# Performance work log

Hardware: AMD Instinct MI355X
Metric: run time of the kernel (lower is better)

Reference implementation:

```python
import jax, jax.numpy as jnp
import numpy as np

S, B, D, E, F = 2048, 2, 1024, 8, 4096


def setup_inputs() -> dict:
    key = jax.random.key(0)
    ks = jax.random.split(key, 6)
    x = jax.random.normal(ks[0], (S, B, D), dtype=jnp.float32)
    w_switch = jax.random.normal(ks[1], (D, E), dtype=jnp.float32) / np.sqrt(D)
    b_switch = jnp.zeros((E,), dtype=jnp.float32)
    w1 = jax.random.normal(ks[2], (E, D, F), dtype=jnp.float32) / np.sqrt(D)
    b1 = jnp.zeros((E, F), dtype=jnp.float32)
    w2 = jax.random.normal(ks[3], (E, F, D), dtype=jnp.float32) / np.sqrt(F)
    b2 = jnp.zeros((E, D), dtype=jnp.float32)
    return {"x": x, "w_switch": w_switch, "b_switch": b_switch,
            "w1": w1, "b1": b1, "w2": w2, "b2": b2}


def reference(x, w_switch, b_switch, w1, b1, w2, b2):
    # x: [S, B, D] -> tokens [N, D]
    s, b, d = x.shape
    n_experts = w1.shape[0]
    xf = x.reshape(-1, d)                                    # [N, D]
    route_prob = jax.nn.softmax(xf @ w_switch + b_switch, axis=-1)  # [N, E]
    route_prob_max = jnp.max(route_prob, axis=-1)            # [N]
    routes = jnp.argmax(route_prob, axis=-1)                 # [N] int
    # is_scale_prob=True: scale token by its routing probability before FFN
    xs = xf * route_prob_max[:, None]                        # [N, D]
    # Per-expert FFN evaluated densely (drop_tokens=False => every token kept),
    # then each token selects its routed expert's output.
    h = jax.nn.relu(jnp.einsum('nd,edf->enf', xs, w1) + b1[:, None, :])  # [E, N, F]
    y = jnp.einsum('enf,efd->end', h, w2) + b2[:, None, :]               # [E, N, D]
    n = xf.shape[0]
    out = y[routes, jnp.arange(n)]                           # [N, D]
    counts = jnp.zeros((n_experts,), dtype=jnp.float32).at[routes].add(1.0)
    n_dropped = jnp.zeros((), dtype=jnp.int32)               # drop_tokens=False
    return out.reshape(s, b, d), counts, route_prob.sum(0), n_dropped
```

## Files before the change

### kernel.cpp

```cpp
#include <hip/hip_runtime.h>
#include <hip/hip_bf16.h>

#define NTOK 4096
#define DDIM 1024
#define NEXP 8
#define FDIM 4096
#define MAXTILES 40

typedef __attribute__((ext_vector_type(4))) float f32x4;
typedef __attribute__((ext_vector_type(8))) short bf16x8;
typedef __attribute__((ext_vector_type(8))) unsigned short u16x8;

#define GLDS(g, l) __builtin_amdgcn_global_load_lds( \
    (const __attribute__((address_space(1))) unsigned int*)(g), \
    (__attribute__((address_space(3))) unsigned int*)(l), 16, 0, 0)

__global__ __launch_bounds__(256) void route_kernel(
    const float* __restrict__ x,
    const float* __restrict__ w_switch,
    const float* __restrict__ b_switch,
    __hip_bfloat16* __restrict__ xs,
    int* __restrict__ amax_arr,
    float* __restrict__ partial)
{
    const int tid = threadIdx.x;
    const int wave = tid >> 6, lane = tid & 63;
    __shared__ float pr[4][16];

    float wacc[16];
#pragma unroll
    for (int j = 0; j < 16; j++) wacc[j] = 0.0f;

    for (int i = 0; i < 4; i++) {
        const int n = blockIdx.x * 16 + wave * 4 + i;
        const float4* xr = (const float4*)(x + (size_t)n * DDIM);
        float4 xv[4];
#pragma unroll
        for (int j = 0; j < 4; j++) xv[j] = xr[lane + j * 64];

        float acc[NEXP];
#pragma unroll
        for (int e = 0; e < NEXP; e++) acc[e] = 0.0f;
#pragma unroll
        for (int j = 0; j < 4; j++) {
            const int dbase = (lane + j * 64) * 4;
#pragma unroll
            for (int c = 0; c < 4; c++) {
                const float4* wr = (const float4*)(w_switch + (size_t)(dbase + c) * NEXP);
                float4 w0 = wr[0], w1 = wr[1];
                float xvc = ((const float*)&xv[j])[c];
                acc[0] += xvc * w0.x; acc[1] += xvc * w0.y;
                acc[2] += xvc * w0.z; acc[3] += xvc * w0.w;
                acc[4] += xvc * w1.x; acc[5] += xvc * w1.y;
                acc[6] += xvc * w1.z; acc[7] += xvc * w1.w;
            }
        }
#pragma unroll
        for (int e = 0; e < NEXP; e++) {
            float v = acc[e];
#pragma unroll
            for (int off = 32; off > 0; off >>= 1) v += __shfl_xor(v, off, 64);
            acc[e] = v;
        }
        float mx = -1e30f;
#pragma unroll
        for (int e = 0; e < NEXP; e++) {
            acc[e] += b_switch[e];
            mx = fmaxf(mx, acc[e]);
        }
        float sum = 0.0f;
#pragma unroll
        for (int e = 0; e < NEXP; e++) { acc[e] = __expf(acc[e] - mx); sum += acc[e]; }
        float inv = 1.0f / sum;
        float pmax = -1.0f; int amax = 0;
#pragma unroll
        for (int e = 0; e < NEXP; e++) {
            float p = acc[e] * inv;
            acc[e] = p;
            if (p > pmax) { pmax = p; amax = e; }
        }
#pragma unroll
        for (int e = 0; e < NEXP; e++) {
            wacc[e] += acc[e];
            wacc[8 + e] += (amax == e) ? 1.0f : 0.0f;
        }
        if (lane == 0) amax_arr[n] = amax;
#pragma unroll
        for (int j = 0; j < 4; j++) {
            ushort4 pk;
            __hip_bfloat16* pp = (__hip_bfloat16*)&pk;
            pp[0] = __float2bfloat16(xv[j].x * pmax);
            pp[1] = __float2bfloat16(xv[j].y * pmax);
            pp[2] = __float2bfloat16(xv[j].z * pmax);
            pp[3] = __float2bfloat16(xv[j].w * pmax);
            *(ushort4*)(xs + (size_t)n * DDIM + (lane + j * 64) * 4) = pk;
        }
    }
    if (lane == 0) {
#pragma unroll
        for (int j = 0; j < 16; j++) pr[wave][j] = wacc[j];
    }
    __syncthreads();
    if (tid < 16)
        partial[blockIdx.x * 16 + tid] = pr[0][tid] + pr[1][tid] + pr[2][tid] + pr[3][tid];
}

__global__ __launch_bounds__(1024) void bucket_kernel(
    const int* __restrict__ amax_arr, int* __restrict__ bucket, int* __restrict__ ecnt)
{
    const int e = blockIdx.x;
    __shared__ int ctr;
    if (threadIdx.x == 0) ctr = 0;
    __syncthreads();
    const int lane = threadIdx.x & 63;
    for (int c = 0; c < NTOK; c += 1024) {
        int t = c + threadIdx.x;
        bool my = (amax_arr[t] == e);
        unsigned long long mask = __ballot(my);
        int cnt = __popcll(mask);
        int base = 0;
        if (lane == 0 && cnt) base = atomicAdd(&ctr, cnt);
        base = __shfl(base, 0, 64);
        if (my) {
            int rank = __popcll(mask & ((1ull << lane) - 1ull));
            bucket[e * NTOK + base + rank] = t;
        }
    }
    __syncthreads();
    if (threadIdx.x == 0) ecnt[e] = ctr;
}

__global__ __launch_bounds__(256) void finalize_table_kernel(
    const float* __restrict__ partial, const int* __restrict__ ecnt,
    float* __restrict__ out_tail, int* __restrict__ table)
{
    __shared__ float red[16][16];
    const int j = threadIdx.x & 15, g = threadIdx.x >> 4;
    float s = 0.0f;
    for (int k = 0; k < 16; k++) s += partial[(size_t)(g + k * 16) * 16 + j];
    red[g][j] = s;
    __syncthreads();
    if (threadIdx.x < 16) {
        float t = 0.0f;
        for (int k = 0; k < 16; k++) t += red[k][threadIdx.x];
        int dst = (threadIdx.x < 8) ? (8 + threadIdx.x) : (threadIdx.x - 8);
        out_tail[dst] = t;
    }
    if (threadIdx.x == 16) out_tail[16] = 0.0f;
    if (threadIdx.x == 0) {
        int idx = 0;
        for (int e = 0; e < NEXP; e++) {
            int cnt = ecnt[e];
            for (int m0 = 0; m0 < cnt; m0 += 128) table[idx++] = (e << 16) | m0;
        }
        for (; idx < MAXTILES; idx++) table[idx] = -1;
    }
}

template <int R, int C>
__global__ __launch_bounds__(256) void transpose_kernel(
    const float* __restrict__ in, __hip_bfloat16* __restrict__ outp)
{
    const int e = blockIdx.z;
    const int r0 = blockIdx.y * 64, c0 = blockIdx.x * 64;
    __shared__ __hip_bfloat16 t[64 * 65];
    const int tid = threadIdx.x;
    const int ri = tid >> 4, c4 = (tid & 15) * 4;
    const float* src = in + ((size_t)e * R + r0) * C + c0;
#pragma unroll
    for (int rr = 0; rr < 4; rr++) {
        int r = ri + rr * 16;
        float4 v = *(const float4*)(src + (size_t)r * C + c4);
        t[r * 65 + c4 + 0] = __float2bfloat16(v.x);
        t[r * 65 + c4 + 1] = __float2bfloat16(v.y);
        t[r * 65 + c4 + 2] = __float2bfloat16(v.z);
        t[r * 65 + c4 + 3] = __float2bfloat16(v.w);
    }
    __syncthreads();
    const int co = tid >> 2, m = tid & 3;
    u16x8 v0, v1;
#pragma unroll
    for (int idx = 0; idx < 8; idx++)
        ((unsigned short*)&v0)[idx] = *(const unsigned short*)&t[(m * 16 + idx) * 65 + co];
#pragma unroll
    for (int idx = 0; idx < 8; idx++)
        ((unsigned short*)&v1)[idx] = *(const unsigned short*)&t[(m * 16 + idx + 8) * 65 + co];
    __hip_bfloat16* dst = outp + ((size_t)e * C + c0 + co) * R + r0 + m * 16;
    *(u16x8*)(dst) = v0;
    *(u16x8*)(dst + 8) = v1;
}

template <int MODE, int K, int NN, int KS, int NX>
__device__ __forceinline__ void gemm_body(
    const __hip_bfloat16* __restrict__ A,
    const __hip_bfloat16* __restrict__ Bt,
    const float* __restrict__ bias,
    const int* __restrict__ bucket,
    const int* __restrict__ ecnt,
    const int* __restrict__ table,
    void* __restrict__ Out)
{
    const int bid = blockIdx.x;
    const int xcd = bid & 7;
    const int q = bid >> 3;
    const int x = q % NX;
    const int yk = (q / NX) % (MAXTILES / 8);
    const int z = q / (NX * (MAXTILES / 8));
    const int y = xcd + 8 * yk;

    const int entry = table[y];
    if (entry < 0) return;
    const int e = entry >> 16;
    const int m0 = entry & 0xffff;
    const int cnt = ecnt[e];
    const int n0 = x * 128;
    const int kbase = (K / KS) * z;

    __shared__ __align__(16) __hip_bfloat16 Asm[128 * 32];
    __shared__ __align__(16) __hip_bfloat16 Bsm[128 * 32];
    __shared__ int toks[128];

    const int tid = threadIdx.x;
    if (tid < 128) {
        int r = m0 + tid;
        toks[tid] = bucket[e * NTOK + (r < cnt ? r : cnt - 1)];
    }
    __syncthreads();

    const int wave = tid >> 6, lane = tid & 63;
    const int r = lane & 15, kq = lane >> 4;
    const int g0 = 2 * wave, g1 = 2 * wave + 1;

    const __hip_bfloat16* pA0 = A + (size_t)toks[g0 * 16 + r] * K + kbase + kq * 8;
    const __hip_bfloat16* pA1 = A + (size_t)toks[g1 * 16 + r] * K + kbase + kq * 8;
    const __hip_bfloat16* pB0 = Bt + ((size_t)e * NN + n0 + g0 * 16 + r) * K + kbase + kq * 8;
    const __hip_bfloat16* pB1 = Bt + ((size_t)e * NN + n0 + g1 * 16 + r) * K + kbase + kq * 8;
    char* lA0 = (char*)Asm + g0 * 1024;
    char* lA1 = (char*)Asm + g1 * 1024;
    char* lB0 = (char*)Bsm + g0 * 1024;
    char* lB1 = (char*)Bsm + g1 * 1024;

    const int wm = wave & 1, wn = wave >> 1;
    f32x4 acc[4][4];
#pragma unroll
    for (int t = 0; t < 4; t++)
#pragma unroll
        for (int u = 0; u < 4; u++) acc[t][u] = (f32x4){0.f, 0.f, 0.f, 0.f};

    for (int k0 = 0; k0 < K / KS; k0 += 32) {
        GLDS(pA0, lA0); GLDS(pA1, lA1);
        GLDS(pB0, lB0); GLDS(pB1, lB1);
        pA0 += 32; pA1 += 32; pB0 += 32; pB1 += 32;
        __syncthreads();
        bf16x8 a[4], b[4];
#pragma unroll
        for (int t = 0; t < 4; t++)
            a[t] = *(const bf16x8*)((const char*)Asm + (wm * 4 + t) * 1024 + lane * 16);
#pragma unroll
        for (int u = 0; u < 4; u++)
            b[u] = *(const bf16x8*)((const char*)Bsm + (wn * 4 + u) * 1024 + lane * 16);
#pragma unroll
        for (int t = 0; t < 4; t++)
#pragma unroll
            for (int u = 0; u < 4; u++)
                acc[t][u] = __builtin_amdgcn_mfma_f32_16x16x32_bf16(a[t], b[u], acc[t][u], 0, 0, 0);
        __syncthreads();
    }

    const int quad = lane >> 4, l15 = lane & 15;
    float bv[4];
#pragma unroll
    for (int u = 0; u < 4; u++) {
        if (MODE == 0)
            bv[u] = bias[(size_t)e * NN + n0 + wn * 64 + u * 16 + l15];
        else
            bv[u] = (z == 0) ? bias[(size_t)e * NN + n0 + wn * 64 + u * 16 + l15] : 0.0f;
    }
#pragma unroll
    for (int t = 0; t < 4; t++) {
#pragma unroll
        for (int rr = 0; rr < 4; rr++) {
            int row = wm * 64 + t * 16 + quad * 4 + rr;
            if (m0 + row < cnt) {
                int tok = toks[row];
#pragma unroll
                for (int u = 0; u < 4; u++) {
                    int col = n0 + wn * 64 + u * 16 + l15;
                    float v = acc[t][u][rr] + bv[u];
                    if (MODE == 0) {
                        v = fmaxf(v, 0.0f);
                        ((__hip_bfloat16*)Out)[(size_t)tok * NN + col] = __float2bfloat16(v);
                    } else {
                        unsafeAtomicAdd(&((float*)Out)[(size_t)tok * NN + col], v);
                    }
                }
            }
        }
    }
}

__global__ __launch_bounds__(256) void gemm_ffn1(
    const __hip_bfloat16* __restrict__ A, const __hip_bfloat16* __restrict__ Bt,
    const float* __restrict__ bias, const int* __restrict__ bucket,
    const int* __restrict__ ecnt, const int* __restrict__ table, void* __restrict__ Out)
{
    gemm_body<0, DDIM, FDIM, 1, FDIM / 128>(A, Bt, bias, bucket, ecnt, table, Out);
}

__global__ __launch_bounds__(256) void gemm_ffn2(
    const __hip_bfloat16* __restrict__ A, const __hip_bfloat16* __restrict__ Bt,
    const float* __restrict__ bias, const int* __restrict__ bucket,
    const int* __restrict__ ecnt, const int* __restrict__ table, void* __restrict__ Out)
{
    gemm_body<1, FDIM, DDIM, 2, DDIM / 128>(A, Bt, bias, bucket, ecnt, table, Out);
}

extern "C" void kernel_launch(void* const* d_in, const int* in_sizes, int n_in,
                              void* d_out, int out_size, void* d_ws, size_t ws_size,
                              hipStream_t stream) {
    const float* x        = (const float*)d_in[0];
    const float* w_switch = (const float*)d_in[1];
    const float* b_switch = (const float*)d_in[2];
    const float* w1       = (const float*)d_in[3];
    const float* b1       = (const float*)d_in[4];
    const float* w2       = (const float*)d_in[5];
    const float* b2       = (const float*)d_in[6];

    float* out = (float*)d_out;
    float* out_tail = out + (size_t)NTOK * DDIM;

    char* ws = (char*)d_ws;
    __hip_bfloat16* xs = (__hip_bfloat16*)(ws);
    __hip_bfloat16* h  = (__hip_bfloat16*)(ws + 8388608ull);
    __hip_bfloat16* wt = (__hip_bfloat16*)(ws + 41943040ull);
    int* bucket        = (int*)(ws + 109051904ull);
    int* amax_arr      = (int*)(ws + 109182976ull);
    float* partial     = (float*)(ws + 109199360ull);
    int* ecnt          = (int*)(ws + 109215744ull);
    int* table         = (int*)(ws + 109215776ull);

    hipMemsetAsync(out, 0, (size_t)NTOK * DDIM * sizeof(float), stream);

    hipLaunchKernelGGL(route_kernel, dim3(256), dim3(256), 0, stream,
                       x, w_switch, b_switch, xs, amax_arr, partial);
    hipLaunchKernelGGL(bucket_kernel, dim3(NEXP), dim3(1024), 0, stream,
                       amax_arr, bucket, ecnt);
    hipLaunchKernelGGL(finalize_table_kernel, dim3(1), dim3(256), 0, stream,
                       partial, ecnt, out_tail, table);

    hipLaunchKernelGGL((transpose_kernel<DDIM, FDIM>), dim3(FDIM / 64, DDIM / 64, NEXP),
                       dim3(256), 0, stream, w1, wt);
    hipLaunchKernelGGL(gemm_ffn1, dim3((FDIM / 128) * MAXTILES), dim3(256), 0, stream,
                       xs, wt, b1, bucket, ecnt, table, (void*)h);

    hipLaunchKernelGGL((transpose_kernel<FDIM, DDIM>), dim3(DDIM / 64, FDIM / 64, NEXP),
                       dim3(256), 0, stream, w2, wt);
    hipLaunchKernelGGL(gemm_ffn2, dim3((DDIM / 128) * MAXTILES * 2), dim3(256), 0, stream,
                       h, wt, b2, bucket, ecnt, table, (void*)out);
}
```

Before: 515.3 us.

## Triple-buffer LDS tiles with async global_load_lds prefetch in expert GEMM

Replaces the single-buffered load/sync/compute loop in the grouped expert GEMM with a three-stage ring of LDS buffers. Loads for step t+2 are issued before computing step t, with manual vmcnt waits and raw s_barrier instead of two __syncthreads per step. LDS fragment reads use inline ds_read_b128 with immediate offsets. This hides global load latency behind MFMA work, at the cost of tripling LDS usage per block, which may reduce occupancy, and of relying on fragile hand-counted waitcnts.

```diff
diff --git a/kernel.cpp b/kernel.cpp
--- a/kernel.cpp
+++ b/kernel.cpp
@@ -14,6 +14,10 @@
 #define GLDS(g, l) __builtin_amdgcn_global_load_lds( \
     (const __attribute__((address_space(1))) unsigned int*)(g), \
     (__attribute__((address_space(3))) unsigned int*)(l), 16, 0, 0)
+
+#define LDSOFF(p) ((unsigned)(unsigned long long)(__attribute__((address_space(3))) char*)(p))
+
+#define DSR(dst, a, o) asm volatile("ds_read_b128 %0, %1 offset:" o : "=v"(dst) : "v"(a))
 
 __global__ __launch_bounds__(256) void route_kernel(
     const float* __restrict__ x,
@@ -216,8 +220,8 @@
     const int n0 = x * 128;
     const int kbase = (K / KS) * z;
 
-    __shared__ __align__(16) __hip_bfloat16 Asm[128 * 32];
-    __shared__ __align__(16) __hip_bfloat16 Bsm[128 * 32];
+    __shared__ __align__(16) __hip_bfloat16 Asm[3][128 * 32];
+    __shared__ __align__(16) __hip_bfloat16 Bsm[3][128 * 32];
     __shared__ int toks[128];
 
     const int tid = threadIdx.x;
@@ -229,42 +233,68 @@
 
     const int wave = tid >> 6, lane = tid & 63;
     const int r = lane & 15, kq = lane >> 4;
-    const int g0 = 2 * wave, g1 = 2 * wave + 1;
+    const int g0 = 2 * wave;
 
     const __hip_bfloat16* pA0 = A + (size_t)toks[g0 * 16 + r] * K + kbase + kq * 8;
-    const __hip_bfloat16* pA1 = A + (size_t)toks[g1 * 16 + r] * K + kbase + kq * 8;
+    const __hip_bfloat16* pA1 = A + (size_t)toks[(g0 + 1) * 16 + r] * K + kbase + kq * 8;
     const __hip_bfloat16* pB0 = Bt + ((size_t)e * NN + n0 + g0 * 16 + r) * K + kbase + kq * 8;
-    const __hip_bfloat16* pB1 = Bt + ((size_t)e * NN + n0 + g1 * 16 + r) * K + kbase + kq * 8;
-    char* lA0 = (char*)Asm + g0 * 1024;
-    char* lA1 = (char*)Asm + g1 * 1024;
-    char* lB0 = (char*)Bsm + g0 * 1024;
-    char* lB1 = (char*)Bsm + g1 * 1024;
+    const __hip_bfloat16* pB1 = Bt + ((size_t)e * NN + n0 + (g0 + 1) * 16 + r) * K + kbase + kq * 8;
 
     const int wm = wave & 1, wn = wave >> 1;
+    const unsigned aBase = LDSOFF((char*)Asm) + wm * 4096 + lane * 16;
+    const unsigned bBase = LDSOFF((char*)Bsm) + wn * 4096 + lane * 16;
+
     f32x4 acc[4][4];
 #pragma unroll
     for (int t = 0; t < 4; t++)
 #pragma unroll
         for (int u = 0; u < 4; u++) acc[t][u] = (f32x4){0.f, 0.f, 0.f, 0.f};
 
-    for (int k0 = 0; k0 < K / KS; k0 += 32) {
-        GLDS(pA0, lA0); GLDS(pA1, lA1);
-        GLDS(pB0, lB0); GLDS(pB1, lB1);
+    constexpr int NSTEP = (K / KS) / 32;
+    static_assert(NSTEP >= 3, "pipeline needs >=3 K-steps");
+
+    auto stage = [&](int b) {
+        char* la = (char*)Asm + b * 8192 + g0 * 1024;
+        char* lb = (char*)Bsm + b * 8192 + g0 * 1024;
+        GLDS(pA0, la); GLDS(pA1, la + 1024);
+        GLDS(pB0, lb); GLDS(pB1, lb + 1024);
         pA0 += 32; pA1 += 32; pB0 += 32; pB1 += 32;
-        __syncthreads();
-        bf16x8 a[4], b[4];
-#pragma unroll
-        for (int t = 0; t < 4; t++)
-            a[t] = *(const bf16x8*)((const char*)Asm + (wm * 4 + t) * 1024 + lane * 16);
-#pragma unroll
-        for (int u = 0; u < 4; u++)
-            b[u] = *(const bf16x8*)((const char*)Bsm + (wn * 4 + u) * 1024 + lane * 16);
-#pragma unroll
-        for (int t = 0; t < 4; t++)
+    };
+
+    stage(0);
+    stage(1);
+    asm volatile("s_waitcnt vmcnt(4)");
+    __builtin_amdgcn_s_barrier();
+
+    int cb = 0, sb = 2;
+    for (int t = 0; t < NSTEP; ++t) {
+        if (t + 2 < NSTEP) stage(sb);
+
+        const unsigned aA = aBase + cb * 8192;
+        const unsigned aB = bBase + cb * 8192;
+        bf16x8 af[4], bf_[4];
+        DSR(af[0], aA, "0");    DSR(af[1], aA, "1024");
+        DSR(af[2], aA, "2048"); DSR(af[3], aA, "3072");
+        DSR(bf_[0], aB, "0");    DSR(bf_[1], aB, "1024");
+        DSR(bf_[2], aB, "2048"); DSR(bf_[3], aB, "3072");
+        asm volatile("s_waitcnt lgkmcnt(0)");
+        __builtin_amdgcn_sched_barrier(0);
+
+#pragma unroll
+        for (int t4 = 0; t4 < 4; t4++)
 #pragma unroll
             for (int u = 0; u < 4; u++)
-                acc[t][u] = __builtin_amdgcn_mfma_f32_16x16x32_bf16(a[t], b[u], acc[t][u], 0, 0, 0);
-        __syncthreads();
+                acc[t4][u] = __builtin_amdgcn_mfma_f32_16x16x32_bf16(af[t4], bf_[u], acc[t4][u], 0, 0, 0);
+
+        if (t + 2 < NSTEP) {
+            asm volatile("s_waitcnt vmcnt(4)");
+            __builtin_amdgcn_s_barrier();
+        } else if (t + 1 < NSTEP) {
+            asm volatile("s_waitcnt vmcnt(0)");
+            __builtin_amdgcn_s_barrier();
+        }
+        cb = (cb == 2) ? 0 : cb + 1;
+        sb = (sb == 2) ? 0 : sb + 1;
     }
 
     const int quad = lane >> 4, l15 = lane & 15;
```

Result: no change. 513.0 us (-0.4%).

## Double GEMM K-tile to 64, row-major LDS staging, split-K 4 for FFN2

Applied to the files above, without the earlier changes.

The grouped expert GEMMs now stage a 64-wide K slice per iteration instead of 32. Each LDS buffer is laid out as 128 rows of 128 bytes, and the MFMA loop runs two sub-steps per barrier pair, which halves the number of __syncthreads per K. The second FFN GEMM raises split-K from 2 to 4 to put more blocks on the device, at the cost of more atomic adds into the fp32 output. Launch bounds now request 4 blocks per SM. The row-major LDS reads at a 128-byte stride may cause bank conflicts that the old fragment-ordered layout avoided.

```diff
diff --git a/kernel.cpp b/kernel.cpp
--- a/kernel.cpp
+++ b/kernel.cpp
@@ -216,8 +216,8 @@
     const int n0 = x * 128;
     const int kbase = (K / KS) * z;
 
-    __shared__ __align__(16) __hip_bfloat16 Asm[128 * 32];
-    __shared__ __align__(16) __hip_bfloat16 Bsm[128 * 32];
+    __shared__ __align__(16) __hip_bfloat16 Asm[128 * 64];
+    __shared__ __align__(16) __hip_bfloat16 Bsm[128 * 64];
     __shared__ int toks[128];
 
     const int tid = threadIdx.x;
@@ -228,42 +228,51 @@
     __syncthreads();
 
     const int wave = tid >> 6, lane = tid & 63;
-    const int r = lane & 15, kq = lane >> 4;
-    const int g0 = 2 * wave, g1 = 2 * wave + 1;
-
-    const __hip_bfloat16* pA0 = A + (size_t)toks[g0 * 16 + r] * K + kbase + kq * 8;
-    const __hip_bfloat16* pA1 = A + (size_t)toks[g1 * 16 + r] * K + kbase + kq * 8;
-    const __hip_bfloat16* pB0 = Bt + ((size_t)e * NN + n0 + g0 * 16 + r) * K + kbase + kq * 8;
-    const __hip_bfloat16* pB1 = Bt + ((size_t)e * NN + n0 + g1 * 16 + r) * K + kbase + kq * 8;
-    char* lA0 = (char*)Asm + g0 * 1024;
-    char* lA1 = (char*)Asm + g1 * 1024;
-    char* lB0 = (char*)Bsm + g0 * 1024;
-    char* lB1 = (char*)Bsm + g1 * 1024;
+    const int srow = lane >> 3;
+    const int scol = (lane & 7) * 16;
+
+    const char* pA[4];
+#pragma unroll
+    for (int i = 0; i < 4; i++)
+        pA[i] = (const char*)(A + (size_t)toks[wave * 32 + i * 8 + srow] * K + kbase) + scol;
+    const char* pB = (const char*)(Bt + ((size_t)e * NN + n0 + wave * 32 + srow) * K + kbase) + scol;
 
     const int wm = wave & 1, wn = wave >> 1;
+    const int r16 = lane & 15, kq16 = lane >> 4;
+
     f32x4 acc[4][4];
 #pragma unroll
     for (int t = 0; t < 4; t++)
 #pragma unroll
         for (int u = 0; u < 4; u++) acc[t][u] = (f32x4){0.f, 0.f, 0.f, 0.f};
 
-    for (int k0 = 0; k0 < K / KS; k0 += 32) {
-        GLDS(pA0, lA0); GLDS(pA1, lA1);
-        GLDS(pB0, lB0); GLDS(pB1, lB1);
-        pA0 += 32; pA1 += 32; pB0 += 32; pB1 += 32;
+    for (int k0 = 0; k0 < K / KS; k0 += 64) {
+#pragma unroll
+        for (int i = 0; i < 4; i++) {
+            GLDS(pA[i], (char*)Asm + (wave * 32 + i * 8) * 128 + lane * 16);
+            GLDS(pB + (size_t)i * 8 * K * 2, (char*)Bsm + (wave * 32 + i * 8) * 128 + lane * 16);
+            pA[i] += 128;
+        }
+        pB += 128;
         __syncthreads();
-        bf16x8 a[4], b[4];
-#pragma unroll
-        for (int t = 0; t < 4; t++)
-            a[t] = *(const bf16x8*)((const char*)Asm + (wm * 4 + t) * 1024 + lane * 16);
-#pragma unroll
-        for (int u = 0; u < 4; u++)
-            b[u] = *(const bf16x8*)((const char*)Bsm + (wn * 4 + u) * 1024 + lane * 16);
-#pragma unroll
-        for (int t = 0; t < 4; t++)
+
+#pragma unroll
+        for (int ksub = 0; ksub < 2; ksub++) {
+            bf16x8 a[4], b[4];
+#pragma unroll
+            for (int t = 0; t < 4; t++)
+                a[t] = *(const bf16x8*)((const char*)Asm +
+                        (wm * 64 + t * 16 + r16) * 128 + kq16 * 16 + ksub * 64);
 #pragma unroll
             for (int u = 0; u < 4; u++)
-                acc[t][u] = __builtin_amdgcn_mfma_f32_16x16x32_bf16(a[t], b[u], acc[t][u], 0, 0, 0);
+                b[u] = *(const bf16x8*)((const char*)Bsm +
+                        (wn * 64 + u * 16 + r16) * 128 + kq16 * 16 + ksub * 64);
+#pragma unroll
+            for (int t = 0; t < 4; t++)
+#pragma unroll
+                for (int u = 0; u < 4; u++)
+                    acc[t][u] = __builtin_amdgcn_mfma_f32_16x16x32_bf16(a[t], b[u], acc[t][u], 0, 0, 0);
+        }
         __syncthreads();
     }
 
@@ -299,7 +308,7 @@
     }
 }
 
-__global__ __launch_bounds__(256) void gemm_ffn1(
+__global__ __launch_bounds__(256, 4) void gemm_ffn1(
     const __hip_bfloat16* __restrict__ A, const __hip_bfloat16* __restrict__ Bt,
     const float* __restrict__ bias, const int* __restrict__ bucket,
     const int* __restrict__ ecnt, const int* __restrict__ table, void* __restrict__ Out)
@@ -307,12 +316,12 @@
     gemm_body<0, DDIM, FDIM, 1, FDIM / 128>(A, Bt, bias, bucket, ecnt, table, Out);
 }
 
-__global__ __launch_bounds__(256) void gemm_ffn2(
+__global__ __launch_bounds__(256, 4) void gemm_ffn2(
     const __hip_bfloat16* __restrict__ A, const __hip_bfloat16* __restrict__ Bt,
     const float* __restrict__ bias, const int* __restrict__ bucket,
     const int* __restrict__ ecnt, const int* __restrict__ table, void* __restrict__ Out)
 {
-    gemm_body<1, FDIM, DDIM, 2, DDIM / 128>(A, Bt, bias, bucket, ecnt, table, Out);
+    gemm_body<1, FDIM, DDIM, 4, DDIM / 128>(A, Bt, bias, bucket, ecnt, table, Out);
 }
 
 extern "C" void kernel_launch(void* const* d_in, const int* in_sizes, int n_in,
@@ -355,6 +364,6 @@
 
     hipLaunchKernelGGL((transpose_kernel<FDIM, DDIM>), dim3(DDIM / 64, FDIM / 64, NEXP),
                        dim3(256), 0, stream, w2, wt);
-    hipLaunchKernelGGL(gemm_ffn2, dim3((DDIM / 128) * MAXTILES * 2), dim3(256), 0, stream,
+    hipLaunchKernelGGL(gemm_ffn2, dim3((DDIM / 128) * MAXTILES * 4), dim3(256), 0, stream,
                        h, wt, b2, bucket, ecnt, table, (void*)out);
 }
```

Measured after the change: 485.3 us. 5.8% less time.
